# Kernel tuning notes

Measured on AMD Instinct MI355X. Metric: run time of the kernel, lower is better.

The kernel has to match this reference:

```python
import jax, jax.numpy as jnp
import numpy as np

ALPHA = 0.3        # Keras LeakyReLU default negative_slope
NUM_STEPS = 16     # fixed-step Dormand-Prince (see notes)
DEPTH = 10
HID = 1024
LOOK = 30
BATCH = 16384


def _leaky(x):
    return jnp.where(x > 0, x, ALPHA * x)


def _mlp(y, W1, b1, W2, b2, W3, b3):
    # drift f(y): 30 -> 1024 -> 1024 -> 30, autonomous (t unused)
    h = _leaky(jnp.dot(y, W1) + b1)
    h = _leaky(jnp.dot(h, W2) + b2)
    return jnp.dot(h, W3) + b3


def _dopri5_step(y, h, params):
    f = lambda z: _mlp(z, *params)
    k1 = f(y)
    k2 = f(y + h * (1.0 / 5.0) * k1)
    k3 = f(y + h * (3.0 / 40.0 * k1 + 9.0 / 40.0 * k2))
    k4 = f(y + h * (44.0 / 45.0 * k1 - 56.0 / 15.0 * k2 + 32.0 / 9.0 * k3))
    k5 = f(y + h * (19372.0 / 6561.0 * k1 - 25360.0 / 2187.0 * k2
                    + 64448.0 / 6561.0 * k3 - 212.0 / 729.0 * k4))
    k6 = f(y + h * (9017.0 / 3168.0 * k1 - 355.0 / 33.0 * k2
                    + 46732.0 / 5247.0 * k3 + 49.0 / 176.0 * k4
                    - 5103.0 / 18656.0 * k5))
    # 5th-order solution (b row of the Dormand-Prince tableau)
    return y + h * (35.0 / 384.0 * k1 + 500.0 / 1113.0 * k3
                    + 125.0 / 192.0 * k4 - 2187.0 / 6784.0 * k5
                    + 11.0 / 84.0 * k6)


def _solve_block(y0, params):
    # integrate dy/dt = f(y) from t=0 to t=1 with fixed step h
    h = 1.0 / NUM_STEPS
    def step(y, _):
        return _dopri5_step(y, h, params), None
    y, _ = jax.lax.scan(step, y0, None, length=NUM_STEPS)
    return y


def setup_inputs() -> dict:
    key = jax.random.key(0)
    ks = jax.random.split(key, 9)
    y0 = jax.random.normal(ks[0], (BATCH, 1, LOOK), dtype=jnp.float32)
    s1 = 1.0 / np.sqrt(LOOK)
    s2 = 1.0 / np.sqrt(HID)
    W1 = jax.random.normal(ks[1], (DEPTH, LOOK, HID), dtype=jnp.float32) * s1
    b1 = jnp.zeros((DEPTH, HID), dtype=jnp.float32)
    W2 = jax.random.normal(ks[2], (DEPTH, HID, HID), dtype=jnp.float32) * s2
    b2 = jnp.zeros((DEPTH, HID), dtype=jnp.float32)
    W3 = jax.random.normal(ks[3], (DEPTH, HID, LOOK), dtype=jnp.float32) * s2
    b3 = jnp.zeros((DEPTH, LOOK), dtype=jnp.float32)
    Wf = jax.random.normal(ks[4], (LOOK, 1), dtype=jnp.float32) * s1
    bf = jnp.zeros((1,), dtype=jnp.float32)
    return {"y0": y0, "W1": W1, "b1": b1, "W2": W2, "b2": b2,
            "W3": W3, "b3": b3, "Wf": Wf, "bf": bf}


def reference(y0, W1, b1, W2, b2, W3, b3, Wf, bf):
    # sequentially apply DEPTH ODE blocks, each with its own drift MLP
    def block(y, p):
        return _solve_block(y, p), None
    y, _ = jax.lax.scan(block, y0, (W1, b1, W2, b2, W3, b3))
    # final readout Dense(output_dim=1)
    return jnp.dot(y, Wf) + bf  # (B, 1, 1)
```

## Files before the change

kernel.cpp:

```cpp
#include <hip/hip_runtime.h>

#define BATCH 16384
#define LOOK 30
#define HID 1024
#define DEPTH 10
#define NSTEPS 16
#define ALPHA 0.3f

typedef short bf16x8 __attribute__((ext_vector_type(8)));
typedef float f32x4 __attribute__((ext_vector_type(4)));

__device__ __forceinline__ float leaky(float x) { return x > 0.f ? x : ALPHA * x; }

__device__ __forceinline__ unsigned short f2bf(float x) {
  unsigned u = __builtin_bit_cast(unsigned, x);
  unsigned r = u + 0x7FFFu + ((u >> 16) & 1u);
  return (unsigned short)(r >> 16);
}
__device__ __forceinline__ float bf2f(unsigned short b) {
  return __builtin_bit_cast(float, (unsigned)b << 16);
}

#define GLD_LDS16(g, l)                                        \
  __builtin_amdgcn_global_load_lds(                            \
      (const __attribute__((address_space(1))) void*)(g),      \
      (__attribute__((address_space(3))) void*)(l), 16, 0, 0)

__global__ __launch_bounds__(256) void k_w2split(const float* __restrict__ W2d,
                                                 short* __restrict__ W2Th,
                                                 short* __restrict__ W2Tl) {
  __shared__ float t[64][65];
  const int kb = blockIdx.x * 64;
  const int nb = blockIdx.y * 64;
  for (int i = threadIdx.x; i < 4096; i += 256) {
    int r = i >> 6, c = i & 63;
    t[r][c] = W2d[(size_t)(kb + r) * HID + nb + c];
  }
  __syncthreads();
  for (int i = threadIdx.x; i < 4096; i += 256) {
    int r = i >> 6, c = i & 63;
    float v = t[c][r];
    unsigned short hi = f2bf(v);
    unsigned short lo = f2bf(v - bf2f(hi));
    W2Th[(size_t)(nb + r) * HID + kb + c] = (short)hi;
    W2Tl[(size_t)(nb + r) * HID + kb + c] = (short)lo;
  }
}

__global__ __launch_bounds__(256) void k_w1t_all(const float* __restrict__ W1,
                                                 short* __restrict__ W1Th,
                                                 short* __restrict__ W1Tl) {
  const int idx = blockIdx.x * 256 + threadIdx.x;
  if (idx >= DEPTH * 1024 * 32) return;
  const int d = idx >> 15;
  const int rem = idx & 32767;
  const int n = rem >> 5, k = rem & 31;
  float v = (k < LOOK) ? W1[(size_t)d * LOOK * HID + (size_t)k * HID + n] : 0.f;
  unsigned short hi = f2bf(v);
  unsigned short lo = f2bf(v - bf2f(hi));
  W1Th[idx] = (short)hi;
  W1Tl[idx] = (short)lo;
}

__global__ __launch_bounds__(256) void k_w3t(const float* __restrict__ W3d,
                                             short* __restrict__ W3Th,
                                             short* __restrict__ W3Tl) {
  const int idx = blockIdx.x * 256 + threadIdx.x;
  if (idx >= 32 * 1024) return;
  const int n = idx >> 10, k = idx & 1023;
  float v = (n < LOOK) ? W3d[(size_t)k * LOOK + n] : 0.f;
  unsigned short hi = f2bf(v);
  unsigned short lo = f2bf(v - bf2f(hi));
  W3Th[idx] = (short)hi;
  W3Tl[idx] = (short)lo;
}

__global__ __launch_bounds__(256) void k_zinit(const float* __restrict__ y0,
                                               short* __restrict__ zh,
                                               short* __restrict__ zl) {
  const int idx = blockIdx.x * 256 + threadIdx.x;
  if (idx >= BATCH * 32) return;
  const int r = idx >> 5, c = idx & 31;
  float v = (c < LOOK) ? y0[(size_t)r * LOOK + c] : 0.f;
  unsigned short hi = f2bf(v);
  unsigned short lo = f2bf(v - bf2f(hi));
  zh[idx] = (short)hi;
  zl[idx] = (short)lo;
}

__global__ __launch_bounds__(512, 2) void k_l1(
    const short* __restrict__ zh, const short* __restrict__ zl,
    const short* __restrict__ W1Th, const short* __restrict__ W1Tl,
    const float* __restrict__ b1d, short* __restrict__ H1h,
    short* __restrict__ H1l) {
  __shared__ short za[2][128 * 32];
  const int tid = threadIdx.x, lane = tid & 63, wave = tid >> 6;
  const int row0 = blockIdx.x * 128;
  const int n0 = blockIdx.y * 256;
  const int wm = wave >> 2, wn = wave & 3;
  const int r15 = lane & 15;
  const int bk = (lane >> 4) * 8;

  bf16x8 bh[4], bl[4];
#pragma unroll
  for (int nj = 0; nj < 4; ++nj) {
    const size_t bo = (size_t)(n0 + wn * 64 + nj * 16 + r15) * 32 + bk;
    bh[nj] = *(const bf16x8*)&W1Th[bo];
    bl[nj] = *(const bf16x8*)&W1Tl[bo];
  }

  GLD_LDS16((const char*)(zh + (size_t)row0 * 32) + tid * 16, &za[0][tid * 8]);
  GLD_LDS16((const char*)(zl + (size_t)row0 * 32) + tid * 16, &za[1][tid * 8]);
  __syncthreads();

  bf16x8 ah[4], al[4];
#pragma unroll
  for (int mi = 0; mi < 4; ++mi) {
    const int ao = (wm * 64 + mi * 16 + r15) * 32 + bk;
    ah[mi] = *(const bf16x8*)&za[0][ao];
    al[mi] = *(const bf16x8*)&za[1][ao];
  }

  f32x4 acc[4][4];
#pragma unroll
  for (int i = 0; i < 4; ++i)
#pragma unroll
    for (int j = 0; j < 4; ++j) acc[i][j] = (f32x4){0.f, 0.f, 0.f, 0.f};

#pragma unroll
  for (int mi = 0; mi < 4; ++mi)
#pragma unroll
    for (int nj = 0; nj < 4; ++nj) {
      acc[mi][nj] = __builtin_amdgcn_mfma_f32_16x16x32_bf16(ah[mi], bh[nj],
                                                            acc[mi][nj], 0, 0, 0);
      acc[mi][nj] = __builtin_amdgcn_mfma_f32_16x16x32_bf16(ah[mi], bl[nj],
                                                            acc[mi][nj], 0, 0, 0);
      acc[mi][nj] = __builtin_amdgcn_mfma_f32_16x16x32_bf16(al[mi], bh[nj],
                                                            acc[mi][nj], 0, 0, 0);
    }

  const int crow = (lane >> 4) * 4;
#pragma unroll
  for (int nj = 0; nj < 4; ++nj) {
    const int col = n0 + wn * 64 + nj * 16 + r15;
    const float bias = b1d[col];
#pragma unroll
    for (int mi = 0; mi < 4; ++mi) {
      const int rb = row0 + wm * 64 + mi * 16 + crow;
#pragma unroll
      for (int r = 0; r < 4; ++r) {
        float v = leaky(acc[mi][nj][r] + bias);
        unsigned short hi = f2bf(v);
        unsigned short lo = f2bf(v - bf2f(hi));
        const size_t o = (size_t)(rb + r) * HID + col;
        H1h[o] = (short)hi;
        H1l[o] = (short)lo;
      }
    }
  }
}

__global__ __launch_bounds__(256, 2) void k_mid(
    const short* __restrict__ H1h, const short* __restrict__ H1l,
    const short* __restrict__ W2Th, const short* __restrict__ W2Tl,
    const float* __restrict__ b2d, short* __restrict__ H2h,
    short* __restrict__ H2l) {
  __shared__ char lds[65536];

  const int tid = threadIdx.x;
  const int lane = tid & 63;
  const int wave = tid >> 6;

  const int bid = blockIdx.x;
  const int wg = (bid & 7) * 128 + (bid >> 3);
  const int mb = wg >> 3, nb = wg & 7;
  const int row0 = mb * 128;
  const int n0 = nb * 128;
  const int wm = wave >> 1;
  const int wnb = wave & 1;
  const int r15 = lane & 15;
  const int kq = lane >> 4;
  const int l7 = lane & 7;
  const int l3 = lane >> 3;

  const char* srcB[8];
  {
    const int s = l7 ^ l3;
    const char* hsrc;
    const char* lsrc;
    int rbase;
    if (wave < 2) {
      hsrc = (const char*)H1h;
      lsrc = (const char*)H1l;
      rbase = row0;
    } else {
      hsrc = (const char*)W2Th;
      lsrc = (const char*)W2Tl;
      rbase = n0;
    }
    const char* base = (s < 4) ? hsrc : lsrc;
    const int w2 = wave & 1;
#pragma unroll
    for (int i = 0; i < 8; ++i) {
      const int c = w2 * 8 + i;
      const int rloc = c * 8 + l3;
      srcB[i] = base + (size_t)(rbase + rloc) * 2048 + (size_t)(s & 3) * 16;
    }
  }
  const int dchunk0 = (wave < 2) ? (wave & 1) * 8192 : 16384 + (wave & 1) * 8192;

  const int offA0 = (wm * 64 + r15) * 128 + ((0 + kq) ^ l7) * 16;
  const int offA1 = (wm * 64 + r15) * 128 + ((4 + kq) ^ l7) * 16;
  const int offB0 = 16384 + (wnb * 64 + r15) * 128 + ((0 + kq) ^ l7) * 16;
  const int offB1 = 16384 + (wnb * 64 + r15) * 128 + ((4 + kq) ^ l7) * 16;

  f32x4 acc[4][4];
#pragma unroll
  for (int i = 0; i < 4; ++i)
#pragma unroll
    for (int j = 0; j < 4; ++j) acc[i][j] = (f32x4){0.f, 0.f, 0.f, 0.f};

#define STAGE(buf, kb)                                                   \
  {                                                                      \
    _Pragma("unroll") for (int i = 0; i < 8; ++i) {                      \
      GLD_LDS16(srcB[i] + (kb), &lds[(buf)*32768 + dchunk0 + i * 1024]); \
    }                                                                    \
  }

  STAGE(0, 0);
  __syncthreads();

  int cur = 0;
  for (int t = 0; t < 32; ++t) {
    if (t < 31) STAGE(cur ^ 1, (t + 1) * 64);

    const char* buf = &lds[cur * 32768];
    bf16x8 bh[4], bl[4];
#pragma unroll
    for (int nj = 0; nj < 4; ++nj) {
      bh[nj] = *(const bf16x8*)(buf + offB0 + nj * 2048);
      bl[nj] = *(const bf16x8*)(buf + offB1 + nj * 2048);
    }
#pragma unroll
    for (int mi = 0; mi < 4; ++mi) {
      bf16x8 ah = *(const bf16x8*)(buf + offA0 + mi * 2048);
      bf16x8 al = *(const bf16x8*)(buf + offA1 + mi * 2048);
#pragma unroll
      for (int nj = 0; nj < 4; ++nj) {
        acc[mi][nj] =
            __builtin_amdgcn_mfma_f32_16x16x32_bf16(ah, bh[nj], acc[mi][nj], 0, 0, 0);
        acc[mi][nj] =
            __builtin_amdgcn_mfma_f32_16x16x32_bf16(ah, bl[nj], acc[mi][nj], 0, 0, 0);
        acc[mi][nj] =
            __builtin_amdgcn_mfma_f32_16x16x32_bf16(al, bh[nj], acc[mi][nj], 0, 0, 0);
      }
    }
    __syncthreads();
    cur ^= 1;
  }
#undef STAGE

  const int crow = (lane >> 4) * 4;
#pragma unroll
  for (int nj = 0; nj < 4; ++nj) {
    const int col = n0 + wnb * 64 + nj * 16 + r15;
    const float bv = b2d[col];
#pragma unroll
    for (int mi = 0; mi < 4; ++mi) {
      const int rb = row0 + wm * 64 + mi * 16 + crow;
#pragma unroll
      for (int r = 0; r < 4; ++r) {
        float v = leaky(acc[mi][nj][r] + bv);
        unsigned short hi = f2bf(v);
        unsigned short lo = f2bf(v - bf2f(hi));
        const size_t o = (size_t)(rb + r) * HID + col;
        H2h[o] = (short)hi;
        H2l[o] = (short)lo;
      }
    }
  }
}

__global__ __launch_bounds__(256, 2) void k_l3l1(
    const short* __restrict__ H2h, const short* __restrict__ H2l,
    const short* __restrict__ W3Th, const short* __restrict__ W3Tl,
    const float* __restrict__ b3d, float* __restrict__ kout,
    const float* __restrict__ K0, const float* __restrict__ K1,
    const float* __restrict__ K2, const float* __restrict__ K3,
    const float* __restrict__ K4, float* __restrict__ y, int combine,
    float p1, float p2, float p3, float p4, float p5, float pc, float hb1,
    float hb2, float hb3, float hb4, float hb5, float hb6,
    const short* __restrict__ W1Tnh, const short* __restrict__ W1Tnl,
    const float* __restrict__ b1n, short* __restrict__ H1h,
    short* __restrict__ H1l) {
  __shared__ short lds[2][4096];
  __shared__ short zs[2][32][40];

  const int tid = threadIdx.x, lane = tid & 63, wave = tid >> 6;
  const int row0 = blockIdx.x * 32;
  const int wm = wave & 1, wn = wave >> 1;

  const int half = tid >> 7;
  const int idx = tid & 127;
  const int srow = idx >> 2;
  const int sd = idx & 3;
  const int slog = sd ^ ((srow >> 1) & 3);
  const short* Asrc = half ? H2l : H2h;
  const short* Bsrc = half ? W3Tl : W3Th;
  const char* aSrc = (const char*)(Asrc + (size_t)(row0 + srow) * HID) + slog * 16;
  const char* bSrc = (const char*)(Bsrc + (size_t)srow * HID) + slog * 16;
  short* aDst0 = &lds[0][half * 1024 + idx * 8];
  short* bDst0 = &lds[0][2048 + half * 1024 + idx * 8];
  short* aDst1 = &lds[1][half * 1024 + idx * 8];
  short* bDst1 = &lds[1][2048 + half * 1024 + idx * 8];

  const int r15 = lane & 15;
  const int kc = lane >> 4;
  const int aRow = wm * 16 + r15;
  const int bRow = wn * 16 + r15;
  const int aOff = aRow * 32 + (kc ^ ((aRow >> 1) & 3)) * 8;
  const int bOff = 2048 + bRow * 32 + (kc ^ ((bRow >> 1) & 3)) * 8;

  f32x4 acc = (f32x4){0.f, 0.f, 0.f, 0.f};

#define STAGE3(ad, bd, kb)          \
  {                                 \
    GLD_LDS16(aSrc + (kb), (ad));   \
    GLD_LDS16(bSrc + (kb), (bd));   \
  }

  STAGE3(aDst0, bDst0, 0);
  __syncthreads();

  for (int t = 0; t < 32; ++t) {
    const int cur = t & 1;
    if (t < 31) {
      if (cur == 0) STAGE3(aDst1, bDst1, (t + 1) * 64)
      else STAGE3(aDst0, bDst0, (t + 1) * 64)
    }
    const short* buf = lds[cur];
    bf16x8 ah = *(const bf16x8*)(buf + aOff);
    bf16x8 al = *(const bf16x8*)(buf + 1024 + aOff);
    bf16x8 bh = *(const bf16x8*)(buf + bOff);
    bf16x8 bl = *(const bf16x8*)(buf + 1024 + bOff);
    acc = __builtin_amdgcn_mfma_f32_16x16x32_bf16(ah, bh, acc, 0, 0, 0);
    acc = __builtin_amdgcn_mfma_f32_16x16x32_bf16(ah, bl, acc, 0, 0, 0);
    acc = __builtin_amdgcn_mfma_f32_16x16x32_bf16(al, bh, acc, 0, 0, 0);
    __syncthreads();
  }
#undef STAGE3

  {
    const int c = wn * 16 + r15;
    const int rb = wm * 16 + (lane >> 4) * 4;
    const float bias = (c < LOOK) ? b3d[c] : 0.f;
#pragma unroll
    for (int r = 0; r < 4; ++r) {
      const int rloc = rb + r;
      const int row = row0 + rloc;
      const float kv = acc[r] + bias;
      float zv = 0.f;
      if (c < LOOK) {
        const size_t id = (size_t)row * LOOK + c;
        const float yv = y[id];
        if (combine) {
          float yn = yv + hb1 * K0[id] + hb2 * K1[id] + hb3 * K2[id] +
                     hb4 * K3[id] + hb5 * K4[id] + hb6 * kv;
          y[id] = yn;
          zv = yn;
        } else {
          kout[id] = kv;
          zv = yv + pc * kv;
          if (p1 != 0.f) zv += p1 * K0[id];
          if (p2 != 0.f) zv += p2 * K1[id];
          if (p3 != 0.f) zv += p3 * K2[id];
          if (p4 != 0.f) zv += p4 * K3[id];
          if (p5 != 0.f) zv += p5 * K4[id];
        }
      }
      unsigned short hi = f2bf(zv);
      unsigned short lo = f2bf(zv - bf2f(hi));
      zs[0][rloc][c] = (short)hi;
      zs[1][rloc][c] = (short)lo;
    }
  }
  __syncthreads();

  bf16x8 zfh[2], zfl[2];
#pragma unroll
  for (int mi = 0; mi < 2; ++mi) {
    zfh[mi] = *(const bf16x8*)&zs[0][mi * 16 + r15][kc * 8];
    zfl[mi] = *(const bf16x8*)&zs[1][mi * 16 + r15][kc * 8];
  }
  const int crow = (lane >> 4) * 4;
#pragma unroll
  for (int nj = 0; nj < 16; ++nj) {
    const int col = wave * 256 + nj * 16 + r15;
    const size_t bo = (size_t)col * 32 + kc * 8;
    bf16x8 bh = *(const bf16x8*)&W1Tnh[bo];
    bf16x8 bl = *(const bf16x8*)&W1Tnl[bo];
    f32x4 a0 = (f32x4){0.f, 0.f, 0.f, 0.f};
    f32x4 a1 = (f32x4){0.f, 0.f, 0.f, 0.f};
    a0 = __builtin_amdgcn_mfma_f32_16x16x32_bf16(zfh[0], bh, a0, 0, 0, 0);
    a0 = __builtin_amdgcn_mfma_f32_16x16x32_bf16(zfh[0], bl, a0, 0, 0, 0);
    a0 = __builtin_amdgcn_mfma_f32_16x16x32_bf16(zfl[0], bh, a0, 0, 0, 0);
    a1 = __builtin_amdgcn_mfma_f32_16x16x32_bf16(zfh[1], bh, a1, 0, 0, 0);
    a1 = __builtin_amdgcn_mfma_f32_16x16x32_bf16(zfh[1], bl, a1, 0, 0, 0);
    a1 = __builtin_amdgcn_mfma_f32_16x16x32_bf16(zfl[1], bh, a1, 0, 0, 0);
    const float bias = b1n[col];
#pragma unroll
    for (int mi = 0; mi < 2; ++mi) {
      const f32x4 av = mi ? a1 : a0;
      const int rbase = row0 + mi * 16 + crow;
#pragma unroll
      for (int r = 0; r < 4; ++r) {
        float v = leaky(av[r] + bias);
        unsigned short hi = f2bf(v);
        unsigned short lo = f2bf(v - bf2f(hi));
        const size_t o = (size_t)(rbase + r) * HID + col;
        H1h[o] = (short)hi;
        H1l[o] = (short)lo;
      }
    }
  }
}

__global__ __launch_bounds__(256) void k_readout(const float* __restrict__ y,
                                                 const float* __restrict__ Wf,
                                                 const float* __restrict__ bf,
                                                 float* __restrict__ out) {
  const int r = blockIdx.x * blockDim.x + threadIdx.x;
  if (r >= BATCH) return;
  float acc = bf[0];
#pragma unroll
  for (int c = 0; c < LOOK; ++c) acc += y[(size_t)r * LOOK + c] * Wf[c];
  out[r] = acc;
}

extern "C" void kernel_launch(void* const* d_in, const int* in_sizes, int n_in,
                              void* d_out, int out_size, void* d_ws,
                              size_t ws_size, hipStream_t stream) {
  const float* y0 = (const float*)d_in[0];
  const float* W1 = (const float*)d_in[1];
  const float* b1 = (const float*)d_in[2];
  const float* W2 = (const float*)d_in[3];
  const float* b2 = (const float*)d_in[4];
  const float* W3 = (const float*)d_in[5];
  const float* b3 = (const float*)d_in[6];
  const float* Wf = (const float*)d_in[7];
  const float* bf = (const float*)d_in[8];
  float* out = (float*)d_out;

  const size_t NY = (size_t)BATCH * LOOK;
  float* f = (float*)d_ws;
  float* y = f;
  float* kk[5];
  for (int i = 0; i < 5; ++i) kk[i] = f + NY * (1 + i);
  char* p = (char*)(f + NY * 6);
  short* zh = (short*)p; p += (size_t)BATCH * 32 * 2;
  short* zl = (short*)p; p += (size_t)BATCH * 32 * 2;
  short* H1h = (short*)p; p += (size_t)BATCH * HID * 2;
  short* H1l = (short*)p; p += (size_t)BATCH * HID * 2;
  short* H2h = (short*)p; p += (size_t)BATCH * HID * 2;
  short* H2l = (short*)p; p += (size_t)BATCH * HID * 2;
  short* W2Th = (short*)p; p += (size_t)HID * HID * 2;
  short* W2Tl = (short*)p; p += (size_t)HID * HID * 2;
  short* W1Th = (short*)p; p += (size_t)DEPTH * HID * 32 * 2;
  short* W1Tl = (short*)p; p += (size_t)DEPTH * HID * 32 * 2;
  short* W3Th = (short*)p; p += (size_t)32 * HID * 2;
  short* W3Tl = (short*)p;

  hipMemcpyAsync(y, y0, NY * sizeof(float), hipMemcpyDeviceToDevice, stream);

  k_w1t_all<<<dim3(DEPTH * 1024 * 32 / 256), 256, 0, stream>>>(W1, W1Th, W1Tl);
  k_zinit<<<dim3(BATCH * 32 / 256), 256, 0, stream>>>(y0, zh, zl);
  k_l1<<<dim3(BATCH / 128, HID / 256), 512, 0, stream>>>(zh, zl, W1Th, W1Tl,
                                                         b1, H1h, H1l);

  const double hh = 1.0 / 16.0;
  static const double A[6][5] = {
      {0, 0, 0, 0, 0},
      {1.0 / 5, 0, 0, 0, 0},
      {3.0 / 40, 9.0 / 40, 0, 0, 0},
      {44.0 / 45, -56.0 / 15, 32.0 / 9, 0, 0},
      {19372.0 / 6561, -25360.0 / 2187, 64448.0 / 6561, -212.0 / 729, 0},
      {9017.0 / 3168, -355.0 / 33, 46732.0 / 5247, 49.0 / 176,
       -5103.0 / 18656},
  };
  static const double Bb[6] = {35.0 / 384,  0,              500.0 / 1113,
                               125.0 / 192, -2187.0 / 6784, 11.0 / 84};

  const float hb1 = (float)(hh * Bb[0]);
  const float hb2 = (float)(hh * Bb[1]);
  const float hb3 = (float)(hh * Bb[2]);
  const float hb4 = (float)(hh * Bb[3]);
  const float hb5 = (float)(hh * Bb[4]);
  const float hb6 = (float)(hh * Bb[5]);

  for (int d = 0; d < DEPTH; ++d) {
    const float* W2d = W2 + (size_t)d * HID * HID;
    const float* b2d = b2 + (size_t)d * HID;
    const float* W3d = W3 + (size_t)d * HID * LOOK;
    const float* b3d = b3 + (size_t)d * LOOK;

    k_w2split<<<dim3(16, 16), 256, 0, stream>>>(W2d, W2Th, W2Tl);
    k_w3t<<<dim3(128), 256, 0, stream>>>(W3d, W3Th, W3Tl);

    for (int s = 0; s < NSTEPS; ++s) {
      for (int st = 0; st < 6; ++st) {
        float pv[5] = {0.f, 0.f, 0.f, 0.f, 0.f};
        float pc = 0.f;
        if (st < 5) {
          for (int jj = 0; jj < 5; ++jj)
            if (jj < st) pv[jj] = (float)(hh * A[st + 1][jj]);
          pc = (float)(hh * A[st + 1][st]);
        }
        int dn = d;
        if (st == 5 && s == NSTEPS - 1) dn = (d + 1 < DEPTH) ? d + 1 : d;
        const short* W1Tnh = W1Th + (size_t)dn * HID * 32;
        const short* W1Tnl = W1Tl + (size_t)dn * HID * 32;
        const float* b1n = b1 + (size_t)dn * HID;

        k_mid<<<dim3(1024), 256, 0, stream>>>(H1h, H1l, W2Th, W2Tl, b2d, H2h,
                                              H2l);
        const int comb = (st == 5) ? 1 : 0;
        float* kout = (st < 5) ? kk[st] : kk[0];
        k_l3l1<<<dim3(BATCH / 32), 256, 0, stream>>>(
            H2h, H2l, W3Th, W3Tl, b3d, kout, kk[0], kk[1], kk[2], kk[3],
            kk[4], y, comb, pv[0], pv[1], pv[2], pv[3], pv[4], pc, hb1, hb2,
            hb3, hb4, hb5, hb6, W1Tnh, W1Tnl, b1n, H1h, H1l);
      }
    }
  }

  k_readout<<<dim3(BATCH / 256), 256, 0, stream>>>(y, Wf, bf, out);
}
```

Before: 130.7 ms.

## Fuse layer-3 projection into hidden GEMM epilogue with split-K partials

The layer-2 GEMM kernel now keeps its 128x128 activation tile in LDS (hi/lo bf16 split, swizzled) and immediately multiplies it by the matching 128-row slice of W3, writing per-N-block partial sums of the 30-wide output. The next kernel sums the 8 partials instead of reloading the full H2 activation from global memory. This removes the write and re-read of two BATCHxHID bf16 buffers per stage. In exchange it adds a small fp32 partial buffer, extra MFMA work and direct global W3 loads in the mid-kernel epilogue, and a different summation order.

```diff
diff --git a/kernel.cpp b/kernel.cpp
--- a/kernel.cpp
+++ b/kernel.cpp
@@ -163,8 +163,8 @@
 __global__ __launch_bounds__(256, 2) void k_mid(
     const short* __restrict__ H1h, const short* __restrict__ H1l,
     const short* __restrict__ W2Th, const short* __restrict__ W2Tl,
-    const float* __restrict__ b2d, short* __restrict__ H2h,
-    short* __restrict__ H2l) {
+    const float* __restrict__ b2d, const short* __restrict__ W3Th,
+    const short* __restrict__ W3Tl, float* __restrict__ kpart) {
   __shared__ char lds[65536];
 
   const int tid = threadIdx.x;
@@ -260,107 +260,118 @@
   }
 #undef STAGE
 
-  const int crow = (lane >> 4) * 4;
 #pragma unroll
   for (int nj = 0; nj < 4; ++nj) {
-    const int col = n0 + wnb * 64 + nj * 16 + r15;
-    const float bv = b2d[col];
+    const int k = wnb * 64 + nj * 16 + r15;
+    const float bv = b2d[n0 + k];
+    const int ksub = k >> 4;
+    const int klo = (k & 15) * 2;
 #pragma unroll
     for (int mi = 0; mi < 4; ++mi) {
-      const int rb = row0 + wm * 64 + mi * 16 + crow;
+      const int rowq = wm * 16 + mi * 4 + kq;
+      const int xr = kq & 3;
+      const int base = (rowq * 8 + ksub) * 128 + klo;
 #pragma unroll
       for (int r = 0; r < 4; ++r) {
         float v = leaky(acc[mi][nj][r] + bv);
         unsigned short hi = f2bf(v);
         unsigned short lo = f2bf(v - bf2f(hi));
-        const size_t o = (size_t)(rb + r) * HID + col;
-        H2h[o] = (short)hi;
-        H2l[o] = (short)lo;
-      }
-    }
-  }
-}
-
-__global__ __launch_bounds__(256, 2) void k_l3l1(
-    const short* __restrict__ H2h, const short* __restrict__ H2l,
-    const short* __restrict__ W3Th, const short* __restrict__ W3Tl,
-    const float* __restrict__ b3d, float* __restrict__ kout,
-    const float* __restrict__ K0, const float* __restrict__ K1,
-    const float* __restrict__ K2, const float* __restrict__ K3,
-    const float* __restrict__ K4, float* __restrict__ y, int combine,
-    float p1, float p2, float p3, float p4, float p5, float pc, float hb1,
-    float hb2, float hb3, float hb4, float hb5, float hb6,
-    const short* __restrict__ W1Tnh, const short* __restrict__ W1Tnl,
-    const float* __restrict__ b1n, short* __restrict__ H1h,
-    short* __restrict__ H1l) {
-  __shared__ short lds[2][4096];
+        const int off = base + ((r ^ xr) & 3) * 32;
+        *(short*)(lds + off) = (short)hi;
+        *(short*)(lds + 32768 + off) = (short)lo;
+      }
+    }
+  }
+  __syncthreads();
+
+  {
+    const int kq8 = kq * 8;
+    f32x4 kacc[2][2];
+#pragma unroll
+    for (int i = 0; i < 2; ++i)
+#pragma unroll
+      for (int j = 0; j < 2; ++j) kacc[i][j] = (f32x4){0.f, 0.f, 0.f, 0.f};
+
+#pragma unroll
+    for (int kt = 0; kt < 4; ++kt) {
+      bf16x8 ah[2], al[2];
+#pragma unroll
+      for (int mii = 0; mii < 2; ++mii) {
+        const int row = wave * 32 + mii * 16 + r15;
+        const int rowq = row >> 2;
+        const int kk = kt * 32 + kq8;
+        const int byteA = (rowq * 8 + (kk >> 4)) * 128 +
+                          (((row & 3) ^ (rowq & 3)) & 3) * 32 + (kk & 15) * 2;
+        ah[mii] = *(const bf16x8*)(lds + byteA);
+        al[mii] = *(const bf16x8*)(lds + 32768 + byteA);
+      }
+#pragma unroll
+      for (int njj = 0; njj < 2; ++njj) {
+        const int col = njj * 16 + r15;
+        const size_t wo = (size_t)col * 1024 + n0 + kt * 32 + kq8;
+        bf16x8 wh = *(const bf16x8*)&W3Th[wo];
+        bf16x8 wl = *(const bf16x8*)&W3Tl[wo];
+#pragma unroll
+        for (int mii = 0; mii < 2; ++mii) {
+          kacc[mii][njj] = __builtin_amdgcn_mfma_f32_16x16x32_bf16(
+              ah[mii], wh, kacc[mii][njj], 0, 0, 0);
+          kacc[mii][njj] = __builtin_amdgcn_mfma_f32_16x16x32_bf16(
+              ah[mii], wl, kacc[mii][njj], 0, 0, 0);
+          kacc[mii][njj] = __builtin_amdgcn_mfma_f32_16x16x32_bf16(
+              al[mii], wh, kacc[mii][njj], 0, 0, 0);
+        }
+      }
+    }
+
+    const int crow2 = kq * 4;
+#pragma unroll
+    for (int njj = 0; njj < 2; ++njj) {
+      const int col = njj * 16 + r15;
+#pragma unroll
+      for (int mii = 0; mii < 2; ++mii) {
+        const int rbase = row0 + wave * 32 + mii * 16 + crow2;
+#pragma unroll
+        for (int r = 0; r < 4; ++r) {
+          kpart[(size_t)nb * ((size_t)BATCH * 32) + (size_t)(rbase + r) * 32 +
+                col] = kacc[mii][njj][r];
+        }
+      }
+    }
+  }
+}
+
+__global__ __launch_bounds__(256, 4) void k_l3l1(
+    const float* __restrict__ kpart, const float* __restrict__ b3d,
+    float* __restrict__ kout, const float* __restrict__ K0,
+    const float* __restrict__ K1, const float* __restrict__ K2,
+    const float* __restrict__ K3, const float* __restrict__ K4,
+    float* __restrict__ y, int combine, float p1, float p2, float p3,
+    float p4, float p5, float pc, float hb1, float hb2, float hb3, float hb4,
+    float hb5, float hb6, const short* __restrict__ W1Tnh,
+    const short* __restrict__ W1Tnl, const float* __restrict__ b1n,
+    short* __restrict__ H1h, short* __restrict__ H1l) {
   __shared__ short zs[2][32][40];
 
   const int tid = threadIdx.x, lane = tid & 63, wave = tid >> 6;
   const int row0 = blockIdx.x * 32;
   const int wm = wave & 1, wn = wave >> 1;
-
-  const int half = tid >> 7;
-  const int idx = tid & 127;
-  const int srow = idx >> 2;
-  const int sd = idx & 3;
-  const int slog = sd ^ ((srow >> 1) & 3);
-  const short* Asrc = half ? H2l : H2h;
-  const short* Bsrc = half ? W3Tl : W3Th;
-  const char* aSrc = (const char*)(Asrc + (size_t)(row0 + srow) * HID) + slog * 16;
-  const char* bSrc = (const char*)(Bsrc + (size_t)srow * HID) + slog * 16;
-  short* aDst0 = &lds[0][half * 1024 + idx * 8];
-  short* bDst0 = &lds[0][2048 + half * 1024 + idx * 8];
-  short* aDst1 = &lds[1][half * 1024 + idx * 8];
-  short* bDst1 = &lds[1][2048 + half * 1024 + idx * 8];
-
   const int r15 = lane & 15;
   const int kc = lane >> 4;
-  const int aRow = wm * 16 + r15;
-  const int bRow = wn * 16 + r15;
-  const int aOff = aRow * 32 + (kc ^ ((aRow >> 1) & 3)) * 8;
-  const int bOff = 2048 + bRow * 32 + (kc ^ ((bRow >> 1) & 3)) * 8;
-
-  f32x4 acc = (f32x4){0.f, 0.f, 0.f, 0.f};
-
-#define STAGE3(ad, bd, kb)          \
-  {                                 \
-    GLD_LDS16(aSrc + (kb), (ad));   \
-    GLD_LDS16(bSrc + (kb), (bd));   \
-  }
-
-  STAGE3(aDst0, bDst0, 0);
-  __syncthreads();
-
-  for (int t = 0; t < 32; ++t) {
-    const int cur = t & 1;
-    if (t < 31) {
-      if (cur == 0) STAGE3(aDst1, bDst1, (t + 1) * 64)
-      else STAGE3(aDst0, bDst0, (t + 1) * 64)
-    }
-    const short* buf = lds[cur];
-    bf16x8 ah = *(const bf16x8*)(buf + aOff);
-    bf16x8 al = *(const bf16x8*)(buf + 1024 + aOff);
-    bf16x8 bh = *(const bf16x8*)(buf + bOff);
-    bf16x8 bl = *(const bf16x8*)(buf + 1024 + bOff);
-    acc = __builtin_amdgcn_mfma_f32_16x16x32_bf16(ah, bh, acc, 0, 0, 0);
-    acc = __builtin_amdgcn_mfma_f32_16x16x32_bf16(ah, bl, acc, 0, 0, 0);
-    acc = __builtin_amdgcn_mfma_f32_16x16x32_bf16(al, bh, acc, 0, 0, 0);
-    __syncthreads();
-  }
-#undef STAGE3
 
   {
     const int c = wn * 16 + r15;
-    const int rb = wm * 16 + (lane >> 4) * 4;
+    const int rb = wm * 16 + kc * 4;
     const float bias = (c < LOOK) ? b3d[c] : 0.f;
 #pragma unroll
     for (int r = 0; r < 4; ++r) {
       const int rloc = rb + r;
       const int row = row0 + rloc;
-      const float kv = acc[r] + bias;
       float zv = 0.f;
       if (c < LOOK) {
+        float kv = bias;
+#pragma unroll
+        for (int nbi = 0; nbi < 8; ++nbi)
+          kv += kpart[(size_t)nbi * ((size_t)BATCH * 32) + (size_t)row * 32 + c];
         const size_t id = (size_t)row * LOOK + c;
         const float yv = y[id];
         if (combine) {
@@ -392,7 +403,7 @@
     zfh[mi] = *(const bf16x8*)&zs[0][mi * 16 + r15][kc * 8];
     zfl[mi] = *(const bf16x8*)&zs[1][mi * 16 + r15][kc * 8];
   }
-  const int crow = (lane >> 4) * 4;
+  const int crow = kc * 4;
 #pragma unroll
   for (int nj = 0; nj < 16; ++nj) {
     const int col = wave * 256 + nj * 16 + r15;
@@ -461,8 +472,7 @@
   short* zl = (short*)p; p += (size_t)BATCH * 32 * 2;
   short* H1h = (short*)p; p += (size_t)BATCH * HID * 2;
   short* H1l = (short*)p; p += (size_t)BATCH * HID * 2;
-  short* H2h = (short*)p; p += (size_t)BATCH * HID * 2;
-  short* H2l = (short*)p; p += (size_t)BATCH * HID * 2;
+  float* kpart = (float*)p; p += (size_t)8 * BATCH * 32 * 4;
   short* W2Th = (short*)p; p += (size_t)HID * HID * 2;
   short* W2Tl = (short*)p; p += (size_t)HID * HID * 2;
   short* W1Th = (short*)p; p += (size_t)DEPTH * HID * 32 * 2;
@@ -521,14 +531,14 @@
         const short* W1Tnl = W1Tl + (size_t)dn * HID * 32;
         const float* b1n = b1 + (size_t)dn * HID;
 
-        k_mid<<<dim3(1024), 256, 0, stream>>>(H1h, H1l, W2Th, W2Tl, b2d, H2h,
-                                              H2l);
+        k_mid<<<dim3(1024), 256, 0, stream>>>(H1h, H1l, W2Th, W2Tl, b2d,
+                                              W3Th, W3Tl, kpart);
         const int comb = (st == 5) ? 1 : 0;
         float* kout = (st < 5) ? kk[st] : kk[0];
         k_l3l1<<<dim3(BATCH / 32), 256, 0, stream>>>(
-            H2h, H2l, W3Th, W3Tl, b3d, kout, kk[0], kk[1], kk[2], kk[3],
-            kk[4], y, comb, pv[0], pv[1], pv[2], pv[3], pv[4], pc, hb1, hb2,
-            hb3, hb4, hb5, hb6, W1Tnh, W1Tnl, b1n, H1h, H1l);
+            kpart, b3d, kout, kk[0], kk[1], kk[2], kk[3], kk[4], y, comb,
+            pv[0], pv[1], pv[2], pv[3], pv[4], pc, hb1, hb2, hb3, hb4, hb5,
+            hb6, W1Tnh, W1Tnl, b1n, H1h, H1l);
       }
     }
   }
```

Result: faster. 114.8 ms (-12.1%).
